# Kernel optimization log

Hardware: AMD Instinct MI355X
Metric: run time of the kernel (lower is better)

Reference implementation:

```python
import jax, jax.numpy as jnp
import numpy as np
from jax import lax

NEG = -1e9
B, H, C, TX, TY = 4, 256, 80, 256, 1024  # batch, hidden, mel bins, text len, mel len


def setup_inputs() -> dict:
    key = jax.random.key(0)
    k = jax.random.split(key, 6)
    en = jax.random.normal(k[0], (B, H, TX), jnp.float32)
    mu = jax.random.normal(k[1], (B, C, TX), jnp.float32)
    log_sigma = 0.1 * jax.random.normal(k[2], (B, C, TX), jnp.float32)
    y = jax.random.normal(k[3], (B, C, TY), jnp.float32)
    x_lengths = jax.random.randint(k[4], (B,), TX // 2, TX + 1, jnp.int32)
    y_lengths = jax.random.randint(k[5], (B,), TY // 2, TY + 1, jnp.int32)
    return {"en": en, "mu": mu, "log_sigma": log_sigma, "y": y,
            "x_lengths": x_lengths, "y_lengths": y_lengths}


def sequence_mask(lengths, max_len):
    return jnp.arange(max_len)[None, :] < lengths[:, None]


def compute_log_probs(mu, log_sigma, y):
    # y: [B,C,Ty] -> [B,1,Ty,C]; mu/log_sigma: [B,C,Tx] -> [B,Tx,1,C]
    yb = jnp.transpose(y, (0, 2, 1))[:, None]
    mub = jnp.transpose(mu, (0, 2, 1))[:, :, None]
    lsb = jnp.transpose(log_sigma, (0, 2, 1))[:, :, None]
    # mse / sigma^2 = (y-mu)^2 * exp(-2*log_sigma); mean over channel dim
    expo = -0.5 * jnp.mean((yb - mub) ** 2 * jnp.exp(-2.0 * lsb), axis=-1)  # [B,Tx,Ty]
    return expo - 0.5 * jnp.mean(lsb, axis=-1)  # broadcast [B,Tx,1] -> [B,Tx,Ty]


def maximum_path(logp, mask, x_lengths, y_lengths):
    """Monotonic alignment search (Glow-TTS Viterbi DP), vectorized over batch."""
    b, tx, ty = logp.shape
    lp = jnp.where(mask > 0, logp, NEG)
    cols = jnp.moveaxis(lp, 2, 0)  # [Ty, B, Tx]
    v0 = jnp.broadcast_to(jnp.where(jnp.arange(tx) == 0, 0.0, NEG), (b, tx)).astype(logp.dtype)

    def fwd(v, col):
        v_shift = jnp.concatenate([jnp.full((b, 1), NEG, v.dtype), v[:, :-1]], axis=1)
        diag = v_shift > v  # come from (x-1, y-1) rather than (x, y-1)
        return col + jnp.maximum(v, v_shift), diag

    _, diags = lax.scan(fwd, v0, cols)  # diags: [Ty, B, Tx] bool

    xs_idx = jnp.arange(tx)

    def bwd(idx, inp):
        yv, dcol = inp
        active = yv < y_lengths  # [B]
        row = (xs_idx[None, :] == idx[:, None]) & active[:, None]
        d = jnp.take_along_axis(dcol, idx[:, None], axis=1)[:, 0]
        idx = jnp.where(active & (idx > 0) & d, idx - 1, idx)
        return idx, row

    _, rows = lax.scan(bwd, x_lengths - 1, (jnp.arange(ty), diags), reverse=True)
    return lax.stop_gradient(jnp.moveaxis(rows, 0, 2).astype(logp.dtype))  # [B,Tx,Ty]


def generate_path(dr, mask):
    # dr: [B,Tx] durations; mask: [B,Tx,Ty]
    ty = mask.shape[-1]
    cum = jnp.cumsum(dr, axis=1)
    pm = (jnp.arange(ty)[None, None, :] < cum[:, :, None]).astype(dr.dtype)
    path = pm - jnp.pad(pm, ((0, 0), (1, 0), (0, 0)))[:, :-1]
    return path * mask


def reference(en, mu, log_sigma, y, x_lengths, y_lengths):
    tx, ty = mu.shape[-1], y.shape[-1]
    x_mask = sequence_mask(x_lengths, tx).astype(jnp.float32)  # [B,Tx]
    y_mask = sequence_mask(y_lengths, ty).astype(jnp.float32)  # [B,Ty]
    attn_mask = x_mask[:, :, None] * y_mask[:, None, :]        # [B,Tx,Ty]
    logp = compute_log_probs(mu, log_sigma, y)
    attn = maximum_path(logp, attn_mask, x_lengths, y_lengths)
    dr_mas = jnp.sum(attn, axis=-1)                            # durations [B,Tx]
    path = generate_path(dr_mas, attn_mask)                    # convert_dr_to_align
    # expand_encoder_outputs: attn^T @ en^T -> [B,H,Ty]
    o_en_ex = jnp.einsum('bxy,bhx->bhy', path, en)
    return o_en_ex, logp, attn, dr_mas
```

## Files before the change

### kernel.cpp

```cpp
#include <hip/hip_runtime.h>
#include <cstdint>
#include <cmath>

#define B_ 4
#define H_ 256
#define C_ 80
#define TX_ 256
#define TY_ 1024
#define NC_ 64
#define NEGF (-1e9f)

#define OFF_LOGP (B_*H_*TY_)
#define OFF_ATTN (OFF_LOGP + B_*TX_*TY_)
#define OFF_DR   (OFF_ATTN + B_*TX_*TY_)

__device__ __forceinline__ float dpp_shr1_negfill_f32(float x) {
  union { float f; int i; } u, o, r;
  u.f = x; o.f = NEGF;
  r.i = __builtin_amdgcn_update_dpp(o.i, u.i, 0x138, 0xf, 0xf, false);
  return r.f;
}

__global__ __launch_bounds__(256) void k_logp(
    const float* __restrict__ mu, const float* __restrict__ ls,
    const float* __restrict__ y, const int* __restrict__ xlp,
    const int* __restrict__ ylp, float* __restrict__ logp_out,
    float* __restrict__ lpT)
{
  const int b  = blockIdx.y;
  const int x0 = blockIdx.x * 4;
  const int tid = threadIdx.x;
  __shared__ double s_w[4][C_];
  __shared__ double s_m1[4][C_];
  __shared__ double s_wm2[4][C_];
  __shared__ double s_lsv[4][C_];
  __shared__ double s_K[4];
  __shared__ double s_t0[4];
  __shared__ float tile[TY_][4];
  for (int i = tid; i < 4 * C_; i += 256) {
    int xi = i / C_, c = i - xi * C_;
    double m = (double)mu[(b * C_ + c) * TX_ + x0 + xi];
    double l = (double)ls[(b * C_ + c) * TX_ + x0 + xi];
    double w = exp(-2.0 * l);
    s_w[xi][c]   = w;
    s_m1[xi][c]  = -2.0 * w * m;
    s_wm2[xi][c] = w * m * m;
    s_lsv[xi][c] = l;
  }
  __syncthreads();
  {
    int xi = tid >> 6, cc = tid & 63;
    double kp = (cc < C_) ? s_wm2[xi][cc] : 0.0;
    double tp = (cc < C_) ? s_lsv[xi][cc] : 0.0;
    if (cc + 64 < C_) { kp += s_wm2[xi][cc + 64]; tp += s_lsv[xi][cc + 64]; }
#pragma unroll
    for (int off = 32; off; off >>= 1) {
      kp += __shfl_down(kp, off);
      tp += __shfl_down(tp, off);
    }
    if (cc == 0) { s_K[xi] = kp; s_t0[xi] = -0.5 * (tp * (1.0 / C_)); }
  }
  __syncthreads();

  const int t0 = tid * 4;
  double acc[4][4];
#pragma unroll
  for (int xi = 0; xi < 4; ++xi)
#pragma unroll
    for (int k = 0; k < 4; ++k) acc[xi][k] = 0.0;

  const float4* yp = (const float4*)(y + (size_t)b * C_ * TY_) + tid;
#pragma unroll 4
  for (int c = 0; c < C_; ++c) {
    float4 yv = yp[c * (TY_ / 4)];
    double y0 = yv.x, y1 = yv.y, y2 = yv.z, y3 = yv.w;
#pragma unroll
    for (int xi = 0; xi < 4; ++xi) {
      double w = s_w[xi][c], m1 = s_m1[xi][c];
      double u0 = fma(w, y0, m1), u1 = fma(w, y1, m1);
      double u2 = fma(w, y2, m1), u3 = fma(w, y3, m1);
      acc[xi][0] = fma(u0, y0, acc[xi][0]);
      acc[xi][1] = fma(u1, y1, acc[xi][1]);
      acc[xi][2] = fma(u2, y2, acc[xi][2]);
      acc[xi][3] = fma(u3, y3, acc[xi][3]);
    }
  }

  const int xlen = xlp[b], ylen = ylp[b];
#pragma unroll
  for (int xi = 0; xi < 4; ++xi) {
    int x = x0 + xi;
    double c0 = s_t0[xi], K = s_K[xi];
    float r[4];
#pragma unroll
    for (int k = 0; k < 4; ++k)
      r[k] = (float)((acc[xi][k] + K) * (-0.5 / C_) + c0);
    *(float4*)&logp_out[((size_t)(b * TX_ + x)) * TY_ + t0] =
        make_float4(r[0], r[1], r[2], r[3]);
    bool xm = x < xlen;
#pragma unroll
    for (int k = 0; k < 4; ++k)
      tile[t0 + k][xi] = (xm && (t0 + k) < ylen) ? r[k] : NEGF;
  }
  __syncthreads();

  float* dst = lpT + (size_t)b * TY_ * TX_ + x0;
  const float4* tp = (const float4*)tile;
#pragma unroll
  for (int k = 0; k < 4; ++k) {
    int t = tid + 256 * k;
    *(float4*)&dst[(size_t)t * TX_] = tp[t];
  }
}

#define PHASE_BAR() \
  asm volatile("s_waitcnt lgkmcnt(0)\n\ts_barrier" ::: "memory")

#define PHASEQ(FL, FC, q)                                                   \
  {                                                                         \
    const int cl = (q) - w;                                                 \
    const int clc = cl < 0 ? 0 : (cl >= NC_ ? NC_ - 1 : cl);                \
    const float* cb = gb + (size_t)clc * 16 * TX_ + tid;                    \
    _Pragma("unroll")                                                       \
    for (int i = 0; i < 16; ++i) FL[i] = cb[i * TX_];    \
    const int cc = (q) - 3 - w;                                             \
    if (cc >= 0 && cc < NC_) {                                              \
      if (cc == 0) { v = (tid == 0) ? 0.0f : NEGF; word = 0u; }             \
      const uint32_t bitbase = 1u << ((cc & 1) << 4);                       \
      float* wr = (lane == 63) ? &bdry[cc & 1][w + 1][0] : &dummy[lane];    \
      const float* bp = &bdry[cc & 1][w][0];                                \
      float bv[16];                                                         \
      *(float4*)&bv[0]  = *(const float4*)(bp);                             \
      *(float4*)&bv[4]  = *(const float4*)(bp + 4);                         \
      *(float4*)&bv[8]  = *(const float4*)(bp + 8);                         \
      *(float4*)&bv[12] = *(const float4*)(bp + 12);                        \
      wr[0] = v;                                                            \
      _Pragma("unroll")                                                     \
      for (int i = 0; i < 16; ++i) {                                        \
        float vl = dpp_shr1_negfill_f32(v);                                 \
        if (amlane0) vl = bv[i];                                            \
        if (vl > v) word |= (bitbase << i);                                 \
        float nv = FC[i] + fmaxf(v, vl);                                    \
        if (i < 15) wr[i + 1] = nv;                                         \
        v = nv;                                                             \
      }                                                                     \
      if (cc & 1) { bits[(cc >> 1) * 256 + tid] = word; word = 0u; }        \
    }                                                                       \
    PHASE_BAR();                                                            \
  }

__global__ __launch_bounds__(256, 1) void k_dp(
    const float* __restrict__ lpT, const int* __restrict__ xlp,
    const int* __restrict__ ylp, float* __restrict__ dr_out,
    int* __restrict__ cum_ws, int* __restrict__ xt_ws)
{
  const int b = blockIdx.x;
  const int tid = threadIdx.x;
  const int lane = tid & 63;
  const int w = tid >> 6;
  __shared__ uint32_t bits[8192];
  __shared__ uint32_t dur[TX_];
  __shared__ float bdry[2][5][16];
  __shared__ float dummy[80];

  const float* gb = lpT + (size_t)b * TY_ * TX_;
  const bool amlane0 = (w > 0) && (lane == 0);

  float v = NEGF;
  uint32_t word = 0;
  float f0[16], f1[16], f2[16], f3[16];

  for (int q = 0; q < 72; q += 4) {
    PHASEQ(f0, f1, q);
    PHASEQ(f1, f2, q + 1);
    PHASEQ(f2, f3, q + 2);
    PHASEQ(f3, f0, q + 3);
  }
  __syncthreads();

  dur[tid] = 0;
  __syncthreads();

  const int xlen = xlp[b], ylen = ylp[b];
  if (tid == 0) {
    int idx = xlen - 1;
    int t = ylen - 1;
    while (t >= 0) {
      if (idx == 0) { dur[0] = (uint32_t)(t + 1); break; }
      int ww = t >> 5, rr = t & 31;
      uint32_t wd = bits[ww * 256 + idx];
      wd &= (rr == 31) ? 0xffffffffu : ((1u << (rr + 1)) - 1u);
      while (wd == 0 && ww > 0) { --ww; wd = bits[ww * 256 + idx]; }
      if (wd == 0) { dur[idx] = (uint32_t)(t + 1); break; }
      int bitpos = 31 - __builtin_clz(wd);
      int tp = (ww << 5) | bitpos;
      dur[idx] = (uint32_t)(t - tp + 1);
      --idx;
      t = tp - 1;
    }
  }
  __syncthreads();

  if (w == 0) {
    uint32_t d0 = dur[4 * lane], d1 = dur[4 * lane + 1];
    uint32_t d2 = dur[4 * lane + 2], d3 = dur[4 * lane + 3];
    uint32_t own = d0 + d1 + d2 + d3;
    uint32_t s = own;
#pragma unroll
    for (int off = 1; off < 64; off <<= 1) {
      uint32_t n = __shfl_up(s, off);
      if (lane >= off) s += n;
    }
    uint32_t base = s - own;
    uint32_t c0 = base + d0, c1 = c0 + d1, c2 = c1 + d2, c3 = c2 + d3;
    int x = 4 * lane;
    cum_ws[b * TX_ + x]     = (int)c0;
    cum_ws[b * TX_ + x + 1] = (int)c1;
    cum_ws[b * TX_ + x + 2] = (int)c2;
    cum_ws[b * TX_ + x + 3] = (int)c3;
    dr_out[b * TX_ + x]     = (float)d0;
    dr_out[b * TX_ + x + 1] = (float)d1;
    dr_out[b * TX_ + x + 2] = (float)d2;
    dr_out[b * TX_ + x + 3] = (float)d3;
    int* xt = xt_ws + b * TY_;
    for (uint32_t t = c0 - d0; t < c0; ++t) xt[t] = x;
    for (uint32_t t = c1 - d1; t < c1; ++t) xt[t] = x + 1;
    for (uint32_t t = c2 - d2; t < c2; ++t) xt[t] = x + 2;
    for (uint32_t t = c3 - d3; t < c3; ++t) xt[t] = x + 3;
  }
}

__global__ __launch_bounds__(256) void k_epi(
    const int* __restrict__ cum_ws, const int* __restrict__ xt_ws,
    const float* __restrict__ en, const int* __restrict__ ylp,
    float* __restrict__ attn, float* __restrict__ oen)
{
  const int b = blockIdx.y, bx = blockIdx.x, tid = threadIdx.x;
  __shared__ float row[TX_];
  if (bx < TX_) {
    const int x = bx;
    int hi = cum_ws[b * TX_ + x];
    int lo = (x > 0) ? cum_ws[b * TX_ + x - 1] : 0;
    int t0 = tid * 4;
    float4 v;
    v.x = (t0     >= lo && t0     < hi) ? 1.f : 0.f;
    v.y = (t0 + 1 >= lo && t0 + 1 < hi) ? 1.f : 0.f;
    v.z = (t0 + 2 >= lo && t0 + 2 < hi) ? 1.f : 0.f;
    v.w = (t0 + 3 >= lo && t0 + 3 < hi) ? 1.f : 0.f;
    *(float4*)&attn[((size_t)(b * TX_ + x)) * TY_ + t0] = v;
  } else {
    const int h = bx - TX_;
    row[tid] = en[((size_t)(b * H_ + h)) * TX_ + tid];
    __syncthreads();
    const int ylen = ylp[b];
    int t0 = tid * 4;
    int4 xi = *(const int4*)&xt_ws[b * TY_ + t0];
    float4 v;
    v.x = (t0     < ylen) ? row[xi.x & (TX_ - 1)] : 0.f;
    v.y = (t0 + 1 < ylen) ? row[xi.y & (TX_ - 1)] : 0.f;
    v.z = (t0 + 2 < ylen) ? row[xi.z & (TX_ - 1)] : 0.f;
    v.w = (t0 + 3 < ylen) ? row[xi.w & (TX_ - 1)] : 0.f;
    *(float4*)&oen[((size_t)(b * H_ + h)) * TY_ + t0] = v;
  }
}

extern "C" void kernel_launch(void* const* d_in, const int* in_sizes, int n_in,
                              void* d_out, int out_size, void* d_ws, size_t ws_size,
                              hipStream_t stream)
{
  const float* en = (const float*)d_in[0];
  const float* mu = (const float*)d_in[1];
  const float* ls = (const float*)d_in[2];
  const float* y  = (const float*)d_in[3];
  const int*   xl = (const int*)d_in[4];
  const int*   yl = (const int*)d_in[5];

  float* out  = (float*)d_out;
  float* oen  = out;
  float* logp = out + OFF_LOGP;
  float* attn = out + OFF_ATTN;
  float* dr   = out + OFF_DR;

  int* cum = (int*)d_ws;
  int* xt  = cum + B_ * TX_;

  k_logp<<<dim3(TX_ / 4, B_),   256, 0, stream>>>(mu, ls, y, xl, yl, logp, attn);
  k_dp  <<<B_,                  256, 0, stream>>>(attn, xl, yl, dr, cum, xt);
  k_epi <<<dim3(TX_ + H_, B_),  256, 0, stream>>>(cum, xt, en, yl, attn, oen);
}
```

Before: 183.8 us.

## Run Viterbi DP in a single wavefront with four text positions per lane

The alignment DP kernel moves from four wavefronts that pipeline column chunks, exchanging boundary values through shared memory and barriers, to one 64-lane wavefront. Each lane holds four consecutive text positions, so the cross-lane shift needs only one DPP move per time step, and no barriers are needed inside the loop. Logp columns are prefetched 16 steps ahead as float4 loads, and the direction bits come from sign-bit arithmetic. The serial chain per step becomes longer (four dependent max/add per lane), in exchange for removing synchronisation and shared-memory traffic.

```diff
diff --git a/kernel.cpp b/kernel.cpp
--- a/kernel.cpp
+++ b/kernel.cpp
@@ -7,7 +7,6 @@
 #define C_ 80
 #define TX_ 256
 #define TY_ 1024
-#define NC_ 64
 #define NEGF (-1e9f)
 
 #define OFF_LOGP (B_*H_*TY_)
@@ -113,72 +112,56 @@
   }
 }
 
-#define PHASE_BAR() \
-  asm volatile("s_waitcnt lgkmcnt(0)\n\ts_barrier" ::: "memory")
-
-#define PHASEQ(FL, FC, q)                                                   \
-  {                                                                         \
-    const int cl = (q) - w;                                                 \
-    const int clc = cl < 0 ? 0 : (cl >= NC_ ? NC_ - 1 : cl);                \
-    const float* cb = gb + (size_t)clc * 16 * TX_ + tid;                    \
-    _Pragma("unroll")                                                       \
-    for (int i = 0; i < 16; ++i) FL[i] = cb[i * TX_];    \
-    const int cc = (q) - 3 - w;                                             \
-    if (cc >= 0 && cc < NC_) {                                              \
-      if (cc == 0) { v = (tid == 0) ? 0.0f : NEGF; word = 0u; }             \
-      const uint32_t bitbase = 1u << ((cc & 1) << 4);                       \
-      float* wr = (lane == 63) ? &bdry[cc & 1][w + 1][0] : &dummy[lane];    \
-      const float* bp = &bdry[cc & 1][w][0];                                \
-      float bv[16];                                                         \
-      *(float4*)&bv[0]  = *(const float4*)(bp);                             \
-      *(float4*)&bv[4]  = *(const float4*)(bp + 4);                         \
-      *(float4*)&bv[8]  = *(const float4*)(bp + 8);                         \
-      *(float4*)&bv[12] = *(const float4*)(bp + 12);                        \
-      wr[0] = v;                                                            \
-      _Pragma("unroll")                                                     \
-      for (int i = 0; i < 16; ++i) {                                        \
-        float vl = dpp_shr1_negfill_f32(v);                                 \
-        if (amlane0) vl = bv[i];                                            \
-        if (vl > v) word |= (bitbase << i);                                 \
-        float nv = FC[i] + fmaxf(v, vl);                                    \
-        if (i < 15) wr[i + 1] = nv;                                         \
-        v = nv;                                                             \
-      }                                                                     \
-      if (cc & 1) { bits[(cc >> 1) * 256 + tid] = word; word = 0u; }        \
-    }                                                                       \
-    PHASE_BAR();                                                            \
-  }
-
-__global__ __launch_bounds__(256, 1) void k_dp(
+__global__ __launch_bounds__(64, 1) void k_dp(
     const float* __restrict__ lpT, const int* __restrict__ xlp,
     const int* __restrict__ ylp, float* __restrict__ dr_out,
     int* __restrict__ cum_ws, int* __restrict__ xt_ws)
 {
   const int b = blockIdx.x;
   const int tid = threadIdx.x;
-  const int lane = tid & 63;
-  const int w = tid >> 6;
-  __shared__ uint32_t bits[8192];
-  __shared__ uint32_t dur[TX_];
-  __shared__ float bdry[2][5][16];
-  __shared__ float dummy[80];
-
-  const float* gb = lpT + (size_t)b * TY_ * TX_;
-  const bool amlane0 = (w > 0) && (lane == 0);
-
-  float v = NEGF;
-  uint32_t word = 0;
-  float f0[16], f1[16], f2[16], f3[16];
-
-  for (int q = 0; q < 72; q += 4) {
-    PHASEQ(f0, f1, q);
-    PHASEQ(f1, f2, q + 1);
-    PHASEQ(f2, f3, q + 2);
-    PHASEQ(f3, f0, q + 3);
-  }
-  __syncthreads();
-
-  dur[tid] = 0;
+  const int lane = tid;
+  __shared__ __align__(16) uint32_t bits[8192];
+  __shared__ __align__(16) uint32_t dur[TX_];
+
+  const float4* gb4 = (const float4*)(lpT + (size_t)b * TY_ * TX_);
+
+  float4 c[16];
+#pragma unroll
+  for (int i = 0; i < 16; ++i)
+    c[i] = gb4[(size_t)i * (TX_ / 4) + lane];
+
+  float v0 = (lane == 0) ? 0.0f : NEGF;
+  float v1 = NEGF, v2 = NEGF, v3 = NEGF;
+  uint32_t w0 = 0, w1 = 0, w2 = 0, w3 = 0;
+
+  for (int g = 0; g < 32; ++g) {
+#pragma unroll
+    for (int u = 0; u < 32; ++u) {
+      const int t = g * 32 + u;
+      float4 col = c[u & 15];
+      int tl = t + 16; tl = (tl > TY_ - 1) ? (TY_ - 1) : tl;
+      c[u & 15] = gb4[(size_t)tl * (TX_ / 4) + lane];
+
+      float sh = dpp_shr1_negfill_f32(v3);
+      float m0 = fmaxf(v0, sh);
+      float m1 = fmaxf(v1, v0);
+      float m2 = fmaxf(v2, v1);
+      float m3 = fmaxf(v3, v2);
+      w0 |= (__float_as_uint(v0 - m0) >> 31) << u;
+      w1 |= (__float_as_uint(v1 - m1) >> 31) << u;
+      w2 |= (__float_as_uint(v2 - m2) >> 31) << u;
+      w3 |= (__float_as_uint(v3 - m3) >> 31) << u;
+      v0 = col.x + m0;
+      v1 = col.y + m1;
+      v2 = col.z + m2;
+      v3 = col.w + m3;
+    }
+    *(uint4*)&bits[g * 256 + 4 * lane] = make_uint4(w0, w1, w2, w3);
+    w0 = w1 = w2 = w3 = 0;
+  }
+  __syncthreads();
+
+  *(uint4*)&dur[4 * tid] = make_uint4(0u, 0u, 0u, 0u);
   __syncthreads();
 
   const int xlen = xlp[b], ylen = ylp[b];
@@ -201,7 +184,7 @@
   }
   __syncthreads();
 
-  if (w == 0) {
+  {
     uint32_t d0 = dur[4 * lane], d1 = dur[4 * lane + 1];
     uint32_t d2 = dur[4 * lane + 2], d3 = dur[4 * lane + 3];
     uint32_t own = d0 + d1 + d2 + d3;
@@ -285,6 +268,6 @@
   int* xt  = cum + B_ * TX_;
 
   k_logp<<<dim3(TX_ / 4, B_),   256, 0, stream>>>(mu, ls, y, xl, yl, logp, attn);
-  k_dp  <<<B_,                  256, 0, stream>>>(attn, xl, yl, dr, cum, xt);
+  k_dp  <<<B_,                   64, 0, stream>>>(attn, xl, yl, dr, cum, xt);
   k_epi <<<dim3(TX_ + H_, B_),  256, 0, stream>>>(cum, xt, en, yl, attn, oen);
 }
```

Result: slower. 192.1 us (+4.6%).
